# Performance work log

Measured on AMD Instinct MI355X. Metric: run time of the kernel, lower is better.

Reference implementation:

```python
import jax, jax.numpy as jnp
import numpy as np

N_NODES = 4096
N_GRAPHS = 32
N = N_NODES * N_GRAPHS          # 131072 total nodes
DEG = 32
E = N * DEG                      # 4194304 edges
IN_CH = 16
OUT_CH = 2
EPS_BN = 1e-5


def setup_inputs() -> dict:
    key = jax.random.key(0)
    ks = jax.random.split(key, 24)
    rn = lambda k, s, scale=0.1: (jax.random.normal(k, s, dtype=jnp.float32) * scale)
    return {
        "x": jax.random.normal(ks[0], (N, IN_CH), dtype=jnp.float32),
        "edge_index": jax.random.randint(ks[1], (2, E), 0, N),
        "edge_attr": jax.random.uniform(ks[2], (E, 3), dtype=jnp.float32),
        # GraphConv1: 16 -> 20  (lin_rel has bias, lin_root has no bias; PyG GraphConv)
        "W_rel1": rn(ks[3], (IN_CH, 20)), "b1": jnp.zeros((20,), jnp.float32), "W_root1": rn(ks[4], (IN_CH, 20)),
        # GraphConv2: 20 -> 20
        "W_rel2": rn(ks[5], (20, 20)), "b2": jnp.zeros((20,), jnp.float32), "W_root2": rn(ks[6], (20, 20)),
        # GraphConv3: 20 -> 1
        "W_rel3": rn(ks[7], (20, 1)), "b3": jnp.zeros((1,), jnp.float32), "W_root3": rn(ks[8], (20, 1)),
        # BatchNorm1d(num_nodes) affine params (channel dim = node index)
        "bn1_g": jnp.ones((N_NODES,), jnp.float32), "bn1_b": jnp.zeros((N_NODES,), jnp.float32),
        "bn2_g": jnp.ones((N_NODES,), jnp.float32), "bn2_b": jnp.zeros((N_NODES,), jnp.float32),
        # fc layers, stored [in, out]
        "fc1_W": rn(ks[9], (N_NODES, 50), 0.02), "fc1_b": jnp.zeros((50,), jnp.float32),
        "fc2_W": rn(ks[10], (50, OUT_CH)), "fc2_b": jnp.zeros((OUT_CH,), jnp.float32),
        "num_graphs": N_GRAPHS,
    }


def _graph_conv(x, src, dst, w, W_rel, b_rel, W_root):
    # PyG GraphConv: out_i = lin_root(x_i) + lin_rel( sum_{j->i} w_ji * x_j )
    msg = x[src] * w[:, None]                              # [E, F] gather + scale
    agg = jax.ops.segment_sum(msg, dst, num_segments=x.shape[0])  # scatter-add
    return agg @ W_rel + b_rel + x @ W_root


def _bn_nodes(h3, gamma, beta):
    # BatchNorm1d(num_nodes) in training mode: h3 is [B, num_nodes, F];
    # normalize per node-channel over (batch, feat), biased variance (torch training).
    mu = jnp.mean(h3, axis=(0, 2), keepdims=True)
    var = jnp.var(h3, axis=(0, 2), keepdims=True)
    hn = (h3 - mu) * jax.lax.rsqrt(var + EPS_BN)
    return hn * gamma[None, :, None] + beta[None, :, None]


def reference(x, edge_index, edge_attr,
              W_rel1, b1, W_root1, W_rel2, b2, W_root2, W_rel3, b3, W_root3,
              bn1_g, bn1_b, bn2_g, bn2_b, fc1_W, fc1_b, fc2_W, fc2_b, num_graphs):
    src, dst = edge_index[0], edge_index[1]
    w = edge_attr[:, 2]
    B = num_graphs

    h = _graph_conv(x, src, dst, w, W_rel1, b1, W_root1)
    h = jax.nn.leaky_relu(h)                                   # slope 0.01, matches torch default
    h = _bn_nodes(h.reshape(B, -1, h.shape[-1]), bn1_g, bn1_b).reshape(-1, h.shape[-1])

    h = _graph_conv(h, src, dst, w, W_rel2, b2, W_root2)
    h = jax.nn.leaky_relu(h)
    h = _bn_nodes(h.reshape(B, -1, h.shape[-1]), bn2_g, bn2_b).reshape(-1, h.shape[-1])

    h = _graph_conv(h, src, dst, w, W_rel3, b3, W_root3)
    h = jax.nn.leaky_relu(h)
    h = h.reshape(B, -1)                                        # [B, num_nodes]

    # per-graph normalization; note: divides by var (not std), var is unbiased (torch.var default)
    eps = 1e-10
    out = (h - jnp.mean(h, axis=1, keepdims=True)) / (jnp.var(h, axis=1, keepdims=True, ddof=1) + eps)
    out = jax.nn.leaky_relu(out @ fc1_W + fc1_b)
    # dropout omitted (eval-mode identity)
    out = out @ fc2_W + fc2_b
    return (out, h)
```

## Files before the change

### kernel.cpp

```cpp
#include <hip/hip_runtime.h>
#include <hip/hip_fp16.h>

#define N_NODES 4096
#define N_GRAPHS 32
#define NTOT (N_NODES * N_GRAPHS)
#define NE (NTOT * 32)
#define C1 16
#define C2 20
#define CAP 72

#define NBUCK 512
#define BSHIFT 8
#define BMASK 255
#define CAPB 8960
#define EPB1 8192

__device__ __forceinline__ float lrelu(float v) { return v > 0.f ? v : 0.01f * v; }

__device__ __forceinline__ unsigned pack_edge(int src, float w) {
    int k = __float2int_rn(w * 32768.f);
    if (k > 32767) k = 32767;
    return (unsigned)src | ((unsigned)k << 17);
}
__device__ __forceinline__ void unpack_edge(unsigned p, int& src, float& w) {
    src = (int)(p & 0x1FFFFu);
    w = (float)(p >> 17) * 3.0517578125e-5f;
}

__device__ __forceinline__ uint4 pack8h(const float* v) {
    union { uint4 u4; __half h[8]; } c;
#pragma unroll
    for (int q = 0; q < 8; q++) c.h[q] = __float2half(v[q]);
    return c.u4;
}
__device__ __forceinline__ uint2 pack4h(const float* v) {
    union { uint2 u2; __half h[4]; } c;
#pragma unroll
    for (int q = 0; q < 4; q++) c.h[q] = __float2half(v[q]);
    return c.u2;
}
__device__ __forceinline__ void fma8(uint4 u, float wv, float* acc) {
    union { uint4 u4; __half2 h2[4]; } c; c.u4 = u;
#pragma unroll
    for (int q = 0; q < 4; q++) {
        float2 f = __half22float2(c.h2[q]);
        acc[2 * q]     += f.x * wv;
        acc[2 * q + 1] += f.y * wv;
    }
}
__device__ __forceinline__ void fma4(uint2 u, float wv, float* acc) {
    union { uint2 u2; __half2 h2[2]; } c; c.u2 = u;
#pragma unroll
    for (int q = 0; q < 2; q++) {
        float2 f = __half22float2(c.h2[q]);
        acc[2 * q]     += f.x * wv;
        acc[2 * q + 1] += f.y * wv;
    }
}
__device__ __forceinline__ void unp8(uint4 u, float* v) {
    union { uint4 u4; __half2 h2[4]; } c; c.u4 = u;
#pragma unroll
    for (int q = 0; q < 4; q++) {
        float2 f = __half22float2(c.h2[q]);
        v[2 * q] = f.x; v[2 * q + 1] = f.y;
    }
}
__device__ __forceinline__ void unp4(uint2 u, float* v) {
    union { uint2 u2; __half2 h2[2]; } c; c.u2 = u;
#pragma unroll
    for (int q = 0; q < 2; q++) {
        float2 f = __half22float2(c.h2[q]);
        v[2 * q] = f.x; v[2 * q + 1] = f.y;
    }
}

__global__ __launch_bounds__(256) void k_part1(const int* __restrict__ ei,
                                               const float* __restrict__ ea,
                                               int* __restrict__ gcur,
                                               uint2* __restrict__ part) {
    __shared__ unsigned lrecA[EPB1];
    __shared__ unsigned char lrecB[EPB1];
    __shared__ int hist[NBUCK], sscan[NBUCK], base[NBUCK], lcur[NBUCK];
    __shared__ int ts[256];
    int t = threadIdx.x;
    hist[t] = 0; hist[t + 256] = 0;
    __syncthreads();
    int eb = blockIdx.x * EPB1;
    int dreg[EPB1 / 256];
#pragma unroll
    for (int i = 0; i < EPB1 / 256; i++) {
        int d = ei[NE + eb + i * 256 + t];
        dreg[i] = d;
        atomicAdd(&hist[d >> BSHIFT], 1);
    }
    __syncthreads();
    int a0 = hist[2 * t], a1 = hist[2 * t + 1];
    ts[t] = a0 + a1;
    __syncthreads();
    for (int d = 1; d < 256; d <<= 1) {
        int v = (t >= d) ? ts[t - d] : 0;
        __syncthreads();
        ts[t] += v;
        __syncthreads();
    }
    int excl = (t == 0) ? 0 : ts[t - 1];
    sscan[2 * t] = excl;
    sscan[2 * t + 1] = excl + a0;
    lcur[2 * t] = excl;
    lcur[2 * t + 1] = excl + a0;
    base[t]       = atomicAdd(&gcur[t], hist[t]);
    base[t + 256] = atomicAdd(&gcur[t + 256], hist[t + 256]);
    __syncthreads();
#pragma unroll
    for (int i = 0; i < EPB1 / 256; i++) {
        int e = eb + i * 256 + t;
        int d = dreg[i];
        int b = d >> BSHIFT;
        int pos = atomicAdd(&lcur[b], 1);
        lrecA[pos] = pack_edge(ei[e], ea[3 * e + 2]);
        lrecB[pos] = (unsigned char)(d & BMASK);
    }
    __syncthreads();
    for (int j = t; j < EPB1; j += 256) {
        int lo = 0, hi = NBUCK - 1;
        while (lo < hi) { int mid = (lo + hi + 1) >> 1; if (sscan[mid] <= j) lo = mid; else hi = mid - 1; }
        int b = lo;
        int dp = base[b] + (j - sscan[b]);
        if (dp < CAPB) part[(size_t)b * CAPB + dp] = make_uint2(lrecA[j], (unsigned)lrecB[j]);
    }
}

__global__ __launch_bounds__(256) void k_part2(const int* __restrict__ gcur,
                                               const uint2* __restrict__ part,
                                               unsigned* __restrict__ slots,
                                               int* __restrict__ cnt) {
    __shared__ unsigned tile[128 * CAP];
    __shared__ int cur[128];
    __shared__ int maxc;
    int t = threadIdx.x;
    if (t < 128) cur[t] = 0;
    if (t == 0) maxc = 0;
    __syncthreads();
    int b = blockIdx.x >> 1;
    int halfsel = blockIdx.x & 1;
    int nbase = (b << BSHIFT) + (halfsel << 7);
    int nrec = gcur[b]; if (nrec > CAPB) nrec = CAPB;
    const uint2* rp = part + (size_t)b * CAPB;
    for (int i = t; i < nrec; i += 256) {
        uint2 r = rp[i];
        int ld = (int)r.y;
        if ((ld >> 7) == halfsel) {
            int l = ld & 127;
            int pos = atomicAdd(&cur[l], 1);
            if (pos < CAP) tile[pos * 128 + l] = r.x;
        }
    }
    __syncthreads();
    if (t < 128) { cnt[nbase + t] = cur[t]; atomicMax(&maxc, cur[t]); }
    __syncthreads();
    int mc = maxc; if (mc > CAP) mc = CAP;
    for (int j = t; j < mc * 128; j += 256) {
        int pos = j >> 7, l = j & 127;
        slots[(size_t)pos * NTOT + nbase + l] = tile[j];
    }
}

__global__ void k_fill_slots(const int* __restrict__ ei, const float* __restrict__ ea,
                             int* __restrict__ cnt, unsigned* __restrict__ slots) {
    int e = blockIdx.x * 256 + threadIdx.x;
    if (e >= NE) return;
    int d = ei[NE + e];
    int pos = atomicAdd(&cnt[d], 1);
    if (pos < CAP) slots[(size_t)pos * NTOT + d] = pack_edge(ei[e], ea[3 * e + 2]);
}

__global__ void k_xcast(const float* __restrict__ x, uint4* __restrict__ xa, uint4* __restrict__ xb) {
    int n = blockIdx.x * 256 + threadIdx.x;
    if (n >= NTOT) return;
    float xr[C1];
    const float4* xp = (const float4*)(x + (size_t)n * C1);
#pragma unroll
    for (int q = 0; q < 4; q++) ((float4*)xr)[q] = xp[q];
    xa[n] = pack8h(xr);
    xb[n] = pack8h(xr + 8);
}

__global__ __launch_bounds__(256) void k_conv1(const float* __restrict__ x,
                        const uint4* __restrict__ xa, const uint4* __restrict__ xb,
                        const unsigned* __restrict__ slots, const int* __restrict__ cnt,
                        const float* __restrict__ Wr, const float* __restrict__ bb,
                        const float* __restrict__ Wo, float* __restrict__ t1) {
    __shared__ float sWr[C1 * C2], sWo[C1 * C2], sb[C2];
    for (int k = threadIdx.x; k < C1 * C2; k += 256) { sWr[k] = Wr[k]; sWo[k] = Wo[k]; }
    if (threadIdx.x < C2) sb[threadIdx.x] = bb[threadIdx.x];
    __syncthreads();
    int n = blockIdx.x * 256 + threadIdx.x;
    int m = cnt[n]; if (m > CAP) m = CAP;
    float acc[C1];
#pragma unroll
    for (int i = 0; i < C1; i++) acc[i] = 0.f;
    {
        int i = 0;
        for (; i + 4 <= m; i += 4) {
            unsigned p0 = __builtin_nontemporal_load(slots + (size_t)(i + 0) * NTOT + n);
            unsigned p1 = __builtin_nontemporal_load(slots + (size_t)(i + 1) * NTOT + n);
            unsigned p2 = __builtin_nontemporal_load(slots + (size_t)(i + 2) * NTOT + n);
            unsigned p3 = __builtin_nontemporal_load(slots + (size_t)(i + 3) * NTOT + n);
            int s0, s1, s2, s3; float w0, w1, w2, w3;
            unpack_edge(p0, s0, w0); unpack_edge(p1, s1, w1);
            unpack_edge(p2, s2, w2); unpack_edge(p3, s3, w3);
            uint4 u0 = xa[s0], u1 = xa[s1], u2 = xa[s2], u3 = xa[s3];
            fma8(u0, w0, acc); fma8(u1, w1, acc); fma8(u2, w2, acc); fma8(u3, w3, acc);
        }
        for (; i < m; i++) {
            unsigned p = __builtin_nontemporal_load(slots + (size_t)i * NTOT + n);
            int s; float w; unpack_edge(p, s, w);
            fma8(xa[s], w, acc);
        }
    }
    {
        int i = 0;
        for (; i + 4 <= m; i += 4) {
            unsigned p0 = __builtin_nontemporal_load(slots + (size_t)(i + 0) * NTOT + n);
            unsigned p1 = __builtin_nontemporal_load(slots + (size_t)(i + 1) * NTOT + n);
            unsigned p2 = __builtin_nontemporal_load(slots + (size_t)(i + 2) * NTOT + n);
            unsigned p3 = __builtin_nontemporal_load(slots + (size_t)(i + 3) * NTOT + n);
            int s0, s1, s2, s3; float w0, w1, w2, w3;
            unpack_edge(p0, s0, w0); unpack_edge(p1, s1, w1);
            unpack_edge(p2, s2, w2); unpack_edge(p3, s3, w3);
            uint4 u0 = xb[s0], u1 = xb[s1], u2 = xb[s2], u3 = xb[s3];
            fma8(u0, w0, acc + 8); fma8(u1, w1, acc + 8); fma8(u2, w2, acc + 8); fma8(u3, w3, acc + 8);
        }
        for (; i < m; i++) {
            unsigned p = __builtin_nontemporal_load(slots + (size_t)i * NTOT + n);
            int s; float w; unpack_edge(p, s, w);
            fma8(xb[s], w, acc + 8);
        }
    }
    float xr[C1];
    const float4* xp = (const float4*)(x + (size_t)n * C1);
#pragma unroll
    for (int q = 0; q < 4; q++) ((float4*)xr)[q] = xp[q];
    float outv[C2];
#pragma unroll
    for (int j = 0; j < C2; j++) {
        float a = sb[j];
#pragma unroll
        for (int i = 0; i < C1; i++) a += acc[i] * sWr[i * C2 + j] + xr[i] * sWo[i * C2 + j];
        outv[j] = lrelu(a);
    }
    float4* op = (float4*)(t1 + (size_t)n * C2);
#pragma unroll
    for (int q = 0; q < 5; q++) op[q] = ((float4*)outv)[q];
}

__global__ void k_stats(const float* __restrict__ t, float* __restrict__ mu, float* __restrict__ rs) {
    int i = blockIdx.x;
    float s = 0.f, ss = 0.f;
    for (int k = threadIdx.x; k < N_GRAPHS * C2; k += 64) {
        int g = k / C2, j = k - g * C2;
        float v = t[((size_t)(g * N_NODES + i)) * C2 + j];
        s += v; ss += v * v;
    }
#pragma unroll
    for (int off = 32; off > 0; off >>= 1) { s += __shfl_down(s, off); ss += __shfl_down(ss, off); }
    if (threadIdx.x == 0) {
        float m = s * (1.f / (N_GRAPHS * C2));
        float var = ss * (1.f / (N_GRAPHS * C2)) - m * m;
        mu[i] = m;
        rs[i] = rsqrtf(var + 1e-5f);
    }
}

__global__ void k_bn_apply(const float* __restrict__ t, const float* __restrict__ mu,
                           const float* __restrict__ rs, const float* __restrict__ gam,
                           const float* __restrict__ bet, uint4* __restrict__ hnA,
                           uint2* __restrict__ hnB) {
    int n = blockIdx.x * 256 + threadIdx.x;
    if (n >= NTOT) return;
    int i = n & (N_NODES - 1);
    float sc = rs[i] * gam[i];
    float sh = bet[i] - mu[i] * sc;
    float v[C2];
    const float4* tp = (const float4*)(t + (size_t)n * C2);
#pragma unroll
    for (int q = 0; q < 5; q++) ((float4*)v)[q] = tp[q];
#pragma unroll
    for (int j = 0; j < C2; j++) v[j] = v[j] * sc + sh;
    hnA[n] = pack8h(v);
    uint2* hp = hnB + (size_t)n * 3;
    hp[0] = pack4h(v + 8);
    hp[1] = pack4h(v + 12);
    hp[2] = pack4h(v + 16);
}

__global__ __launch_bounds__(256) void k_conv2(const uint4* __restrict__ hnA,
                        const uint2* __restrict__ hnB,
                        const unsigned* __restrict__ slots, const int* __restrict__ cnt,
                        const float* __restrict__ Wr, const float* __restrict__ bb,
                        const float* __restrict__ Wo, float* __restrict__ t2) {
    __shared__ float sWr[C2 * C2], sWo[C2 * C2], sb[C2];
    for (int k = threadIdx.x; k < C2 * C2; k += 256) { sWr[k] = Wr[k]; sWo[k] = Wo[k]; }
    if (threadIdx.x < C2) sb[threadIdx.x] = bb[threadIdx.x];
    __syncthreads();
    int n = blockIdx.x * 256 + threadIdx.x;
    int m = cnt[n]; if (m > CAP) m = CAP;
    float acc[C2];
#pragma unroll
    for (int i = 0; i < C2; i++) acc[i] = 0.f;
    {
        int i = 0;
        for (; i + 4 <= m; i += 4) {
            unsigned p0 = __builtin_nontemporal_load(slots + (size_t)(i + 0) * NTOT + n);
            unsigned p1 = __builtin_nontemporal_load(slots + (size_t)(i + 1) * NTOT + n);
            unsigned p2 = __builtin_nontemporal_load(slots + (size_t)(i + 2) * NTOT + n);
            unsigned p3 = __builtin_nontemporal_load(slots + (size_t)(i + 3) * NTOT + n);
            int s0, s1, s2, s3; float w0, w1, w2, w3;
            unpack_edge(p0, s0, w0); unpack_edge(p1, s1, w1);
            unpack_edge(p2, s2, w2); unpack_edge(p3, s3, w3);
            uint4 u0 = hnA[s0], u1 = hnA[s1], u2 = hnA[s2], u3 = hnA[s3];
            fma8(u0, w0, acc); fma8(u1, w1, acc); fma8(u2, w2, acc); fma8(u3, w3, acc);
        }
        for (; i < m; i++) {
            unsigned p = __builtin_nontemporal_load(slots + (size_t)i * NTOT + n);
            int s; float w; unpack_edge(p, s, w);
            fma8(hnA[s], w, acc);
        }
    }
    {
        int i = 0;
        for (; i + 4 <= m; i += 4) {
            unsigned p0 = __builtin_nontemporal_load(slots + (size_t)(i + 0) * NTOT + n);
            unsigned p1 = __builtin_nontemporal_load(slots + (size_t)(i + 1) * NTOT + n);
            unsigned p2 = __builtin_nontemporal_load(slots + (size_t)(i + 2) * NTOT + n);
            unsigned p3 = __builtin_nontemporal_load(slots + (size_t)(i + 3) * NTOT + n);
            int s0, s1, s2, s3; float w0, w1, w2, w3;
            unpack_edge(p0, s0, w0); unpack_edge(p1, s1, w1);
            unpack_edge(p2, s2, w2); unpack_edge(p3, s3, w3);
            const uint2* r0 = hnB + (size_t)s0 * 3;
            const uint2* r1 = hnB + (size_t)s1 * 3;
            const uint2* r2 = hnB + (size_t)s2 * 3;
            const uint2* r3 = hnB + (size_t)s3 * 3;
            uint2 a0 = r0[0], b0 = r0[1], c0 = r0[2];
            uint2 a1 = r1[0], b1 = r1[1], c1 = r1[2];
            uint2 a2 = r2[0], b2 = r2[1], c2 = r2[2];
            uint2 a3 = r3[0], b3 = r3[1], c3 = r3[2];
            fma4(a0, w0, acc + 8); fma4(b0, w0, acc + 12); fma4(c0, w0, acc + 16);
            fma4(a1, w1, acc + 8); fma4(b1, w1, acc + 12); fma4(c1, w1, acc + 16);
            fma4(a2, w2, acc + 8); fma4(b2, w2, acc + 12); fma4(c2, w2, acc + 16);
            fma4(a3, w3, acc + 8); fma4(b3, w3, acc + 12); fma4(c3, w3, acc + 16);
        }
        for (; i < m; i++) {
            unsigned p = __builtin_nontemporal_load(slots + (size_t)i * NTOT + n);
            int s; float w; unpack_edge(p, s, w);
            const uint2* r = hnB + (size_t)s * 3;
            fma4(r[0], w, acc + 8); fma4(r[1], w, acc + 12); fma4(r[2], w, acc + 16);
        }
    }
    float h[C2];
    unp8(hnA[n], h);
    {
        const uint2* r = hnB + (size_t)n * 3;
        unp4(r[0], h + 8); unp4(r[1], h + 12); unp4(r[2], h + 16);
    }
    float outv[C2];
#pragma unroll
    for (int j = 0; j < C2; j++) {
        float a = sb[j];
#pragma unroll
        for (int i = 0; i < C2; i++) a += acc[i] * sWr[i * C2 + j] + h[i] * sWo[i * C2 + j];
        outv[j] = lrelu(a);
    }
    float4* op = (float4*)(t2 + (size_t)n * C2);
#pragma unroll
    for (int q = 0; q < 5; q++) op[q] = ((float4*)outv)[q];
}

__global__ void k_bn2_proj(const float* __restrict__ t, const float* __restrict__ mu,
                           const float* __restrict__ rs, const float* __restrict__ gam,
                           const float* __restrict__ bet, const float* __restrict__ Wr3,
                           const float* __restrict__ b3, const float* __restrict__ Wo3,
                           float* __restrict__ y, float* __restrict__ r2) {
    __shared__ float sWr[C2], sWo[C2];
    if (threadIdx.x < C2) { sWr[threadIdx.x] = Wr3[threadIdx.x]; sWo[threadIdx.x] = Wo3[threadIdx.x]; }
    __syncthreads();
    int n = blockIdx.x * 256 + threadIdx.x;
    if (n >= NTOT) return;
    int i = n & (N_NODES - 1);
    float sc = rs[i] * gam[i];
    float sh = bet[i] - mu[i] * sc;
    float v[C2];
    const float4* tp = (const float4*)(t + (size_t)n * C2);
#pragma unroll
    for (int q = 0; q < 5; q++) ((float4*)v)[q] = tp[q];
    float ay = 0.f, ar = 0.f;
#pragma unroll
    for (int j = 0; j < C2; j++) {
        float hv = v[j] * sc + sh;
        ay += hv * sWr[j];
        ar += hv * sWo[j];
    }
    y[n] = ay;
    r2[n] = ar + b3[0];
}

__global__ __launch_bounds__(256) void k_conv3(const float* __restrict__ y, const float* __restrict__ r2,
                        const unsigned* __restrict__ slots, const int* __restrict__ cnt,
                        float* __restrict__ hout, float* __restrict__ gsum, float* __restrict__ gss) {
    __shared__ float ls[4], lss[4];
    int n = blockIdx.x * 256 + threadIdx.x;
    int m = cnt[n]; if (m > CAP) m = CAP;
    float a = 0.f;
    int i = 0;
    for (; i + 4 <= m; i += 4) {
        unsigned p0 = __builtin_nontemporal_load(slots + (size_t)(i + 0) * NTOT + n);
        unsigned p1 = __builtin_nontemporal_load(slots + (size_t)(i + 1) * NTOT + n);
        unsigned p2 = __builtin_nontemporal_load(slots + (size_t)(i + 2) * NTOT + n);
        unsigned p3 = __builtin_nontemporal_load(slots + (size_t)(i + 3) * NTOT + n);
        int s0, s1, s2, s3; float w0, w1, w2, w3;
        unpack_edge(p0, s0, w0); unpack_edge(p1, s1, w1);
        unpack_edge(p2, s2, w2); unpack_edge(p3, s3, w3);
        a += y[s0] * w0 + y[s1] * w1 + y[s2] * w2 + y[s3] * w3;
    }
    for (; i < m; i++) {
        unsigned p = __builtin_nontemporal_load(slots + (size_t)i * NTOT + n);
        int s; float w; unpack_edge(p, s, w);
        a += y[s] * w;
    }
    float v = lrelu(a + r2[n]);
    hout[n] = v;
    float s = v, ss = v * v;
#pragma unroll
    for (int o = 32; o > 0; o >>= 1) { s += __shfl_down(s, o); ss += __shfl_down(ss, o); }
    int wid = threadIdx.x >> 6, lid = threadIdx.x & 63;
    if (lid == 0) { ls[wid] = s; lss[wid] = ss; }
    __syncthreads();
    if (threadIdx.x == 0) {
        int g = blockIdx.x >> 4;
        atomicAdd(&gsum[g], ls[0] + ls[1] + ls[2] + ls[3]);
        atomicAdd(&gss[g], lss[0] + lss[1] + lss[2] + lss[3]);
    }
}

__global__ void k_fc1(const float* __restrict__ h, const float* __restrict__ gsum,
                      const float* __restrict__ gss, const float* __restrict__ W,
                      const float* __restrict__ b, float* __restrict__ z) {
    __shared__ float ls[4];
    int blk = blockIdx.x;
    int g = blk / 50, k = blk - g * 50;
    float mu = gsum[g] / N_NODES;
    float var = (gss[g] - N_NODES * mu * mu) / (N_NODES - 1);
    float inv = 1.f / (var + 1e-10f);
    const float* hr = h + (size_t)g * N_NODES;
    float p = 0.f;
    for (int n = threadIdx.x; n < N_NODES; n += 256)
        p += (hr[n] - mu) * inv * W[(size_t)n * 50 + k];
#pragma unroll
    for (int off = 32; off > 0; off >>= 1) p += __shfl_down(p, off);
    int wid = threadIdx.x >> 6, lid = threadIdx.x & 63;
    if (lid == 0) ls[wid] = p;
    __syncthreads();
    if (threadIdx.x == 0) {
        float S = ls[0] + ls[1] + ls[2] + ls[3];
        z[g * 50 + k] = lrelu(S + b[k]);
    }
}

__global__ void k_fc2(const float* __restrict__ z, const float* __restrict__ W,
                      const float* __restrict__ b, float* __restrict__ out) {
    int t = threadIdx.x;
    if (t >= N_GRAPHS * 2) return;
    int g = t >> 1, o = t & 1;
    float acc = b[o];
#pragma unroll
    for (int k = 0; k < 50; k++) acc += z[g * 50 + k] * W[k * 2 + o];
    out[g * 2 + o] = acc;
}

extern "C" void kernel_launch(void* const* d_in, const int* in_sizes, int n_in,
                              void* d_out, int out_size, void* d_ws, size_t ws_size,
                              hipStream_t stream) {
    const float* x    = (const float*)d_in[0];
    const int*   ei   = (const int*)d_in[1];
    const float* ea   = (const float*)d_in[2];
    const float* Wr1  = (const float*)d_in[3];
    const float* b1   = (const float*)d_in[4];
    const float* Wo1  = (const float*)d_in[5];
    const float* Wr2  = (const float*)d_in[6];
    const float* b2   = (const float*)d_in[7];
    const float* Wo2  = (const float*)d_in[8];
    const float* Wr3  = (const float*)d_in[9];
    const float* b3   = (const float*)d_in[10];
    const float* Wo3  = (const float*)d_in[11];
    const float* bn1g = (const float*)d_in[12];
    const float* bn1b = (const float*)d_in[13];
    const float* bn2g = (const float*)d_in[14];
    const float* bn2b = (const float*)d_in[15];
    const float* fc1W = (const float*)d_in[16];
    const float* fc1b = (const float*)d_in[17];
    const float* fc2W = (const float*)d_in[18];
    const float* fc2b = (const float*)d_in[19];
    float* out = (float*)d_out;

    const size_t part_bytes  = (size_t)NBUCK * CAPB * sizeof(uint2);
    const size_t slots_bytes = (size_t)NTOT * CAP * sizeof(unsigned);
    const size_t tail_bytes  = (size_t)NTOT * C2 * sizeof(float)
                             + (size_t)NTOT * 16 * 3
                             + (size_t)NTOT * 24
                             + (size_t)NTOT * 2 * sizeof(float)
                             + (size_t)NTOT * sizeof(int)
                             + (size_t)(NBUCK + 4 * N_NODES + 8 * N_GRAPHS + N_GRAPHS * 50 + 64) * sizeof(float);
    const bool useSort = ws_size >= part_bytes + slots_bytes + tail_bytes;

    char* wsb = (char*)d_ws;
    uint2*    part  = (uint2*)wsb;     wsb += useSort ? part_bytes : 0;
    unsigned* slots = (unsigned*)wsb;  wsb += slots_bytes;
    float*    bufA  = (float*)wsb;     wsb += (size_t)NTOT * C2 * sizeof(float);
    uint4*    xa    = (uint4*)wsb;     wsb += (size_t)NTOT * 16;
    uint4*    xb    = (uint4*)wsb;     wsb += (size_t)NTOT * 16;
    uint4*    hnA   = (uint4*)wsb;     wsb += (size_t)NTOT * 16;
    uint2*    hnB   = (uint2*)wsb;     wsb += (size_t)NTOT * 24;
    float*    yv    = (float*)wsb;     wsb += (size_t)NTOT * sizeof(float);
    float*    r2v   = (float*)wsb;     wsb += (size_t)NTOT * sizeof(float);
    int*      cnt   = (int*)wsb;       wsb += (size_t)NTOT * sizeof(int);
    int*      gcur  = (int*)wsb;       wsb += NBUCK * sizeof(int);
    float*    mu1   = (float*)wsb;     wsb += N_NODES * sizeof(float);
    float*    rs1   = (float*)wsb;     wsb += N_NODES * sizeof(float);
    float*    mu2   = (float*)wsb;     wsb += N_NODES * sizeof(float);
    float*    rs2   = (float*)wsb;     wsb += N_NODES * sizeof(float);
    float*    gsum  = (float*)wsb;     wsb += N_GRAPHS * sizeof(float);
    float*    gss   = (float*)wsb;     wsb += N_GRAPHS * sizeof(float);
    float*    z     = (float*)wsb;     wsb += N_GRAPHS * 50 * sizeof(float);

    const int EB = (NE + 255) / 256;
    const int NB = (NTOT + 255) / 256;

    hipMemsetAsync(gsum, 0, 2 * N_GRAPHS * sizeof(float), stream);
    k_xcast<<<NB, 256, 0, stream>>>(x, xa, xb);
    if (useSort) {
        hipMemsetAsync(gcur, 0, NBUCK * sizeof(int), stream);
        k_part1<<<NE / EPB1, 256, 0, stream>>>(ei, ea, gcur, part);
        k_part2<<<NBUCK * 2, 256, 0, stream>>>(gcur, part, slots, cnt);
    } else {
        hipMemsetAsync(cnt, 0, (size_t)NTOT * sizeof(int), stream);
        k_fill_slots<<<EB, 256, 0, stream>>>(ei, ea, cnt, slots);
    }

    k_conv1<<<NB, 256, 0, stream>>>(x, xa, xb, slots, cnt, Wr1, b1, Wo1, bufA);
    k_stats<<<N_NODES, 64, 0, stream>>>(bufA, mu1, rs1);
    k_bn_apply<<<NB, 256, 0, stream>>>(bufA, mu1, rs1, bn1g, bn1b, hnA, hnB);

    k_conv2<<<NB, 256, 0, stream>>>(hnA, hnB, slots, cnt, Wr2, b2, Wo2, bufA);
    k_stats<<<N_NODES, 64, 0, stream>>>(bufA, mu2, rs2);
    k_bn2_proj<<<NB, 256, 0, stream>>>(bufA, mu2, rs2, bn2g, bn2b, Wr3, b3, Wo3, yv, r2v);

    k_conv3<<<NB, 256, 0, stream>>>(yv, r2v, slots, cnt, out + 64, gsum, gss);

    k_fc1<<<N_GRAPHS * 50, 256, 0, stream>>>(out + 64, gsum, gss, fc1W, fc1b, z);
    k_fc2<<<1, 64, 0, stream>>>(z, fc2W, fc2b, out);
}
```

Before: 433.1 us.

## Refine bucket partition, pre-extract quantized weights, unroll gathers by eight

Splits the edge partition into 1024 buckets of 128 nodes, so the second pass no longer has two blocks each reading a bucket and discarding half the records. A separate kernel quantizes the edge weights to 16 bits first, so the partition kernel stops doing a strided read of edge_attr. The binary search now reuses the local cursors in place of a separate scan array, and all conv gather loops are unrolled to 8 outstanding loads. Conv1 reads the root features from the fp16 copies instead of fp32 x, which adds rounding error. The extra kernel launch and the higher register pressure from deeper unrolling are the costs.

```diff
diff --git a/kernel.cpp b/kernel.cpp
--- a/kernel.cpp
+++ b/kernel.cpp
@@ -9,18 +9,21 @@
 #define C2 20
 #define CAP 72
 
-#define NBUCK 512
-#define BSHIFT 8
-#define BMASK 255
-#define CAPB 8960
+#define NBUCK 1024
+#define BSHIFT 7
+#define BMASK 127
+#define CAPB 4480
 #define EPB1 8192
 
 __device__ __forceinline__ float lrelu(float v) { return v > 0.f ? v : 0.01f * v; }
 
-__device__ __forceinline__ unsigned pack_edge(int src, float w) {
+__device__ __forceinline__ unsigned short quant_w(float w) {
     int k = __float2int_rn(w * 32768.f);
     if (k > 32767) k = 32767;
-    return (unsigned)src | ((unsigned)k << 17);
+    return (unsigned short)k;
+}
+__device__ __forceinline__ unsigned pack_edge(int src, float w) {
+    return (unsigned)src | ((unsigned)quant_w(w) << 17);
 }
 __device__ __forceinline__ void unpack_edge(unsigned p, int& src, float& w) {
     src = (int)(p & 0x1FFFFu);
@@ -74,16 +77,23 @@
     }
 }
 
+__global__ void k_wext(const float* __restrict__ ea, unsigned short* __restrict__ w16) {
+    int e = blockIdx.x * 256 + threadIdx.x;
+    if (e >= NE) return;
+    w16[e] = quant_w(ea[3 * e + 2]);
+}
+
 __global__ __launch_bounds__(256) void k_part1(const int* __restrict__ ei,
-                                               const float* __restrict__ ea,
+                                               const unsigned short* __restrict__ w16,
                                                int* __restrict__ gcur,
                                                uint2* __restrict__ part) {
     __shared__ unsigned lrecA[EPB1];
     __shared__ unsigned char lrecB[EPB1];
-    __shared__ int hist[NBUCK], sscan[NBUCK], base[NBUCK], lcur[NBUCK];
+    __shared__ int hist[NBUCK], lcur[NBUCK], base[NBUCK];
     __shared__ int ts[256];
     int t = threadIdx.x;
-    hist[t] = 0; hist[t + 256] = 0;
+#pragma unroll
+    for (int q = 0; q < 4; q++) hist[t + q * 256] = 0;
     __syncthreads();
     int eb = blockIdx.x * EPB1;
     int dreg[EPB1 / 256];
@@ -94,8 +104,9 @@
         atomicAdd(&hist[d >> BSHIFT], 1);
     }
     __syncthreads();
-    int a0 = hist[2 * t], a1 = hist[2 * t + 1];
-    ts[t] = a0 + a1;
+    int h0 = hist[4 * t], h1 = hist[4 * t + 1], h2 = hist[4 * t + 2], h3 = hist[4 * t + 3];
+    int lsum = h0 + h1 + h2 + h3;
+    ts[t] = lsum;
     __syncthreads();
     for (int d = 1; d < 256; d <<= 1) {
         int v = (t >= d) ? ts[t - d] : 0;
@@ -104,12 +115,15 @@
         __syncthreads();
     }
     int excl = (t == 0) ? 0 : ts[t - 1];
-    sscan[2 * t] = excl;
-    sscan[2 * t + 1] = excl + a0;
-    lcur[2 * t] = excl;
-    lcur[2 * t + 1] = excl + a0;
-    base[t]       = atomicAdd(&gcur[t], hist[t]);
-    base[t + 256] = atomicAdd(&gcur[t + 256], hist[t + 256]);
+    lcur[4 * t] = excl;
+    lcur[4 * t + 1] = excl + h0;
+    lcur[4 * t + 2] = excl + h0 + h1;
+    lcur[4 * t + 3] = excl + h0 + h1 + h2;
+#pragma unroll
+    for (int q = 0; q < 4; q++) {
+        int b = t + q * 256;
+        base[b] = atomicAdd(&gcur[b], hist[b]);
+    }
     __syncthreads();
 #pragma unroll
     for (int i = 0; i < EPB1 / 256; i++) {
@@ -117,15 +131,16 @@
         int d = dreg[i];
         int b = d >> BSHIFT;
         int pos = atomicAdd(&lcur[b], 1);
-        lrecA[pos] = pack_edge(ei[e], ea[3 * e + 2]);
+        lrecA[pos] = (unsigned)ei[e] | ((unsigned)w16[e] << 17);
         lrecB[pos] = (unsigned char)(d & BMASK);
     }
     __syncthreads();
     for (int j = t; j < EPB1; j += 256) {
-        int lo = 0, hi = NBUCK - 1;
-        while (lo < hi) { int mid = (lo + hi + 1) >> 1; if (sscan[mid] <= j) lo = mid; else hi = mid - 1; }
+        int lo = 0, hi = NBUCK;
+        while (lo < hi) { int mid = (lo + hi) >> 1; if (lcur[mid] <= j) lo = mid + 1; else hi = mid; }
         int b = lo;
-        int dp = base[b] + (j - sscan[b]);
+        int start = (b == 0) ? 0 : lcur[b - 1];
+        int dp = base[b] + (j - start);
         if (dp < CAPB) part[(size_t)b * CAPB + dp] = make_uint2(lrecA[j], (unsigned)lrecB[j]);
     }
 }
@@ -141,19 +156,15 @@
     if (t < 128) cur[t] = 0;
     if (t == 0) maxc = 0;
     __syncthreads();
-    int b = blockIdx.x >> 1;
-    int halfsel = blockIdx.x & 1;
-    int nbase = (b << BSHIFT) + (halfsel << 7);
+    int b = blockIdx.x;
+    int nbase = b << BSHIFT;
     int nrec = gcur[b]; if (nrec > CAPB) nrec = CAPB;
     const uint2* rp = part + (size_t)b * CAPB;
     for (int i = t; i < nrec; i += 256) {
         uint2 r = rp[i];
-        int ld = (int)r.y;
-        if ((ld >> 7) == halfsel) {
-            int l = ld & 127;
-            int pos = atomicAdd(&cur[l], 1);
-            if (pos < CAP) tile[pos * 128 + l] = r.x;
-        }
+        int l = (int)r.y;
+        int pos = atomicAdd(&cur[l], 1);
+        if (pos < CAP) tile[pos * 128 + l] = r.x;
     }
     __syncthreads();
     if (t < 128) { cnt[nbase + t] = cur[t]; atomicMax(&maxc, cur[t]); }
@@ -185,8 +196,7 @@
     xb[n] = pack8h(xr + 8);
 }
 
-__global__ __launch_bounds__(256) void k_conv1(const float* __restrict__ x,
-                        const uint4* __restrict__ xa, const uint4* __restrict__ xb,
+__global__ __launch_bounds__(256) void k_conv1(const uint4* __restrict__ xa, const uint4* __restrict__ xb,
                         const unsigned* __restrict__ slots, const int* __restrict__ cnt,
                         const float* __restrict__ Wr, const float* __restrict__ bb,
                         const float* __restrict__ Wo, float* __restrict__ t1) {
@@ -201,16 +211,15 @@
     for (int i = 0; i < C1; i++) acc[i] = 0.f;
     {
         int i = 0;
-        for (; i + 4 <= m; i += 4) {
-            unsigned p0 = __builtin_nontemporal_load(slots + (size_t)(i + 0) * NTOT + n);
-            unsigned p1 = __builtin_nontemporal_load(slots + (size_t)(i + 1) * NTOT + n);
-            unsigned p2 = __builtin_nontemporal_load(slots + (size_t)(i + 2) * NTOT + n);
-            unsigned p3 = __builtin_nontemporal_load(slots + (size_t)(i + 3) * NTOT + n);
-            int s0, s1, s2, s3; float w0, w1, w2, w3;
-            unpack_edge(p0, s0, w0); unpack_edge(p1, s1, w1);
-            unpack_edge(p2, s2, w2); unpack_edge(p3, s3, w3);
-            uint4 u0 = xa[s0], u1 = xa[s1], u2 = xa[s2], u3 = xa[s3];
-            fma8(u0, w0, acc); fma8(u1, w1, acc); fma8(u2, w2, acc); fma8(u3, w3, acc);
+        for (; i + 8 <= m; i += 8) {
+            unsigned p[8];
+#pragma unroll
+            for (int k = 0; k < 8; k++) p[k] = __builtin_nontemporal_load(slots + (size_t)(i + k) * NTOT + n);
+            uint4 u[8]; float w[8];
+#pragma unroll
+            for (int k = 0; k < 8; k++) { int s; unpack_edge(p[k], s, w[k]); u[k] = xa[s]; }
+#pragma unroll
+            for (int k = 0; k < 8; k++) fma8(u[k], w[k], acc);
         }
         for (; i < m; i++) {
             unsigned p = __builtin_nontemporal_load(slots + (size_t)i * NTOT + n);
@@ -220,16 +229,15 @@
     }
     {
         int i = 0;
-        for (; i + 4 <= m; i += 4) {
-            unsigned p0 = __builtin_nontemporal_load(slots + (size_t)(i + 0) * NTOT + n);
-            unsigned p1 = __builtin_nontemporal_load(slots + (size_t)(i + 1) * NTOT + n);
-            unsigned p2 = __builtin_nontemporal_load(slots + (size_t)(i + 2) * NTOT + n);
-            unsigned p3 = __builtin_nontemporal_load(slots + (size_t)(i + 3) * NTOT + n);
-            int s0, s1, s2, s3; float w0, w1, w2, w3;
-            unpack_edge(p0, s0, w0); unpack_edge(p1, s1, w1);
-            unpack_edge(p2, s2, w2); unpack_edge(p3, s3, w3);
-            uint4 u0 = xb[s0], u1 = xb[s1], u2 = xb[s2], u3 = xb[s3];
-            fma8(u0, w0, acc + 8); fma8(u1, w1, acc + 8); fma8(u2, w2, acc + 8); fma8(u3, w3, acc + 8);
+        for (; i + 8 <= m; i += 8) {
+            unsigned p[8];
+#pragma unroll
+            for (int k = 0; k < 8; k++) p[k] = __builtin_nontemporal_load(slots + (size_t)(i + k) * NTOT + n);
+            uint4 u[8]; float w[8];
+#pragma unroll
+            for (int k = 0; k < 8; k++) { int s; unpack_edge(p[k], s, w[k]); u[k] = xb[s]; }
+#pragma unroll
+            for (int k = 0; k < 8; k++) fma8(u[k], w[k], acc + 8);
         }
         for (; i < m; i++) {
             unsigned p = __builtin_nontemporal_load(slots + (size_t)i * NTOT + n);
@@ -238,9 +246,7 @@
         }
     }
     float xr[C1];
-    const float4* xp = (const float4*)(x + (size_t)n * C1);
-#pragma unroll
-    for (int q = 0; q < 4; q++) ((float4*)xr)[q] = xp[q];
+    unp8(xa[n], xr); unp8(xb[n], xr + 8);
     float outv[C2];
 #pragma unroll
     for (int j = 0; j < C2; j++) {
@@ -310,16 +316,15 @@
     for (int i = 0; i < C2; i++) acc[i] = 0.f;
     {
         int i = 0;
-        for (; i + 4 <= m; i += 4) {
-            unsigned p0 = __builtin_nontemporal_load(slots + (size_t)(i + 0) * NTOT + n);
-            unsigned p1 = __builtin_nontemporal_load(slots + (size_t)(i + 1) * NTOT + n);
-            unsigned p2 = __builtin_nontemporal_load(slots + (size_t)(i + 2) * NTOT + n);
-            unsigned p3 = __builtin_nontemporal_load(slots + (size_t)(i + 3) * NTOT + n);
-            int s0, s1, s2, s3; float w0, w1, w2, w3;
-            unpack_edge(p0, s0, w0); unpack_edge(p1, s1, w1);
-            unpack_edge(p2, s2, w2); unpack_edge(p3, s3, w3);
-            uint4 u0 = hnA[s0], u1 = hnA[s1], u2 = hnA[s2], u3 = hnA[s3];
-            fma8(u0, w0, acc); fma8(u1, w1, acc); fma8(u2, w2, acc); fma8(u3, w3, acc);
+        for (; i + 8 <= m; i += 8) {
+            unsigned p[8];
+#pragma unroll
+            for (int k = 0; k < 8; k++) p[k] = __builtin_nontemporal_load(slots + (size_t)(i + k) * NTOT + n);
+            uint4 u[8]; float w[8];
+#pragma unroll
+            for (int k = 0; k < 8; k++) { int s; unpack_edge(p[k], s, w[k]); u[k] = hnA[s]; }
+#pragma unroll
+            for (int k = 0; k < 8; k++) fma8(u[k], w[k], acc);
         }
         for (; i < m; i++) {
             unsigned p = __builtin_nontemporal_load(slots + (size_t)i * NTOT + n);
@@ -329,26 +334,23 @@
     }
     {
         int i = 0;
-        for (; i + 4 <= m; i += 4) {
-            unsigned p0 = __builtin_nontemporal_load(slots + (size_t)(i + 0) * NTOT + n);
-            unsigned p1 = __builtin_nontemporal_load(slots + (size_t)(i + 1) * NTOT + n);
-            unsigned p2 = __builtin_nontemporal_load(slots + (size_t)(i + 2) * NTOT + n);
-            unsigned p3 = __builtin_nontemporal_load(slots + (size_t)(i + 3) * NTOT + n);
-            int s0, s1, s2, s3; float w0, w1, w2, w3;
-            unpack_edge(p0, s0, w0); unpack_edge(p1, s1, w1);
-            unpack_edge(p2, s2, w2); unpack_edge(p3, s3, w3);
-            const uint2* r0 = hnB + (size_t)s0 * 3;
-            const uint2* r1 = hnB + (size_t)s1 * 3;
-            const uint2* r2 = hnB + (size_t)s2 * 3;
-            const uint2* r3 = hnB + (size_t)s3 * 3;
-            uint2 a0 = r0[0], b0 = r0[1], c0 = r0[2];
-            uint2 a1 = r1[0], b1 = r1[1], c1 = r1[2];
-            uint2 a2 = r2[0], b2 = r2[1], c2 = r2[2];
-            uint2 a3 = r3[0], b3 = r3[1], c3 = r3[2];
-            fma4(a0, w0, acc + 8); fma4(b0, w0, acc + 12); fma4(c0, w0, acc + 16);
-            fma4(a1, w1, acc + 8); fma4(b1, w1, acc + 12); fma4(c1, w1, acc + 16);
-            fma4(a2, w2, acc + 8); fma4(b2, w2, acc + 12); fma4(c2, w2, acc + 16);
-            fma4(a3, w3, acc + 8); fma4(b3, w3, acc + 12); fma4(c3, w3, acc + 16);
+        for (; i + 8 <= m; i += 8) {
+            unsigned p[8];
+#pragma unroll
+            for (int k = 0; k < 8; k++) p[k] = __builtin_nontemporal_load(slots + (size_t)(i + k) * NTOT + n);
+            int s[8]; float w[8];
+#pragma unroll
+            for (int k = 0; k < 8; k++) unpack_edge(p[k], s[k], w[k]);
+            uint2 ua[8], ub[8], uc[8];
+#pragma unroll
+            for (int k = 0; k < 8; k++) {
+                const uint2* r = hnB + (size_t)s[k] * 3;
+                ua[k] = r[0]; ub[k] = r[1]; uc[k] = r[2];
+            }
+#pragma unroll
+            for (int k = 0; k < 8; k++) {
+                fma4(ua[k], w[k], acc + 8); fma4(ub[k], w[k], acc + 12); fma4(uc[k], w[k], acc + 16);
+            }
         }
         for (; i < m; i++) {
             unsigned p = __builtin_nontemporal_load(slots + (size_t)i * NTOT + n);
@@ -412,15 +414,15 @@
     int m = cnt[n]; if (m > CAP) m = CAP;
     float a = 0.f;
     int i = 0;
-    for (; i + 4 <= m; i += 4) {
-        unsigned p0 = __builtin_nontemporal_load(slots + (size_t)(i + 0) * NTOT + n);
-        unsigned p1 = __builtin_nontemporal_load(slots + (size_t)(i + 1) * NTOT + n);
-        unsigned p2 = __builtin_nontemporal_load(slots + (size_t)(i + 2) * NTOT + n);
-        unsigned p3 = __builtin_nontemporal_load(slots + (size_t)(i + 3) * NTOT + n);
-        int s0, s1, s2, s3; float w0, w1, w2, w3;
-        unpack_edge(p0, s0, w0); unpack_edge(p1, s1, w1);
-        unpack_edge(p2, s2, w2); unpack_edge(p3, s3, w3);
-        a += y[s0] * w0 + y[s1] * w1 + y[s2] * w2 + y[s3] * w3;
+    for (; i + 8 <= m; i += 8) {
+        unsigned p[8];
+#pragma unroll
+        for (int k = 0; k < 8; k++) p[k] = __builtin_nontemporal_load(slots + (size_t)(i + k) * NTOT + n);
+        float yv[8]; float w[8];
+#pragma unroll
+        for (int k = 0; k < 8; k++) { int s; unpack_edge(p[k], s, w[k]); yv[k] = y[s]; }
+#pragma unroll
+        for (int k = 0; k < 8; k++) a += yv[k] * w[k];
     }
     for (; i < m; i++) {
         unsigned p = __builtin_nontemporal_load(slots + (size_t)i * NTOT + n);
@@ -507,6 +509,7 @@
     const size_t tail_bytes  = (size_t)NTOT * C2 * sizeof(float)
                              + (size_t)NTOT * 16 * 3
                              + (size_t)NTOT * 24
+                             + (size_t)NE * sizeof(unsigned short)
                              + (size_t)NTOT * 2 * sizeof(float)
                              + (size_t)NTOT * sizeof(int)
                              + (size_t)(NBUCK + 4 * N_NODES + 8 * N_GRAPHS + N_GRAPHS * 50 + 64) * sizeof(float);
@@ -520,6 +523,7 @@
     uint4*    xb    = (uint4*)wsb;     wsb += (size_t)NTOT * 16;
     uint4*    hnA   = (uint4*)wsb;     wsb += (size_t)NTOT * 16;
     uint2*    hnB   = (uint2*)wsb;     wsb += (size_t)NTOT * 24;
+    unsigned short* w16 = (unsigned short*)wsb; wsb += (size_t)NE * sizeof(unsigned short);
     float*    yv    = (float*)wsb;     wsb += (size_t)NTOT * sizeof(float);
     float*    r2v   = (float*)wsb;     wsb += (size_t)NTOT * sizeof(float);
     int*      cnt   = (int*)wsb;       wsb += (size_t)NTOT * sizeof(int);
@@ -539,14 +543,15 @@
     k_xcast<<<NB, 256, 0, stream>>>(x, xa, xb);
     if (useSort) {
         hipMemsetAsync(gcur, 0, NBUCK * sizeof(int), stream);
-        k_part1<<<NE / EPB1, 256, 0, stream>>>(ei, ea, gcur, part);
-        k_part2<<<NBUCK * 2, 256, 0, stream>>>(gcur, part, slots, cnt);
+        k_wext<<<EB, 256, 0, stream>>>(ea, w16);
+        k_part1<<<NE / EPB1, 256, 0, stream>>>(ei, w16, gcur, part);
+        k_part2<<<NBUCK, 256, 0, stream>>>(gcur, part, slots, cnt);
     } else {
         hipMemsetAsync(cnt, 0, (size_t)NTOT * sizeof(int), stream);
         k_fill_slots<<<EB, 256, 0, stream>>>(ei, ea, cnt, slots);
     }
 
-    k_conv1<<<NB, 256, 0, stream>>>(x, xa, xb, slots, cnt, Wr1, b1, Wo1, bufA);
+    k_conv1<<<NB, 256, 0, stream>>>(xa, xb, slots, cnt, Wr1, b1, Wo1, bufA);
     k_stats<<<N_NODES, 64, 0, stream>>>(bufA, mu1, rs1);
     k_bn_apply<<<NB, 256, 0, stream>>>(bufA, mu1, rs1, bn1g, bn1b, hnA, hnB);
 
```

Result: no change. 438.4 us (+1.2%).
